# Optimization experiments

Hardware: AMD Instinct MI355X
Metric: run time of the kernel (lower is better)

The kernel has to match this reference:

```python
import jax, jax.numpy as jnp
import numpy as np

N_NODES = 10000
N_EDGES = 160000
N_GRAPHS = 16
NODE_F = 64
EDGE_F = 32
H = 256
OUT = 512
L = 3


def setup_inputs() -> dict:
    key = jax.random.key(0)
    ks = iter(jax.random.split(key, 64))
    def rn(shape, s=0.05):
        return jax.random.normal(next(ks), shape, dtype=jnp.float32) * s
    f32 = jnp.float32
    inp = {}
    inp["node_features"] = jax.random.normal(next(ks), (N_NODES, NODE_F), dtype=f32)
    inp["edge_index"] = jax.random.randint(next(ks), (2, N_EDGES), 0, N_NODES)
    inp["edge_features"] = jax.random.normal(next(ks), (N_EDGES, EDGE_F), dtype=f32)
    inp["batch"] = jnp.sort(jax.random.randint(next(ks), (N_NODES,), 0, N_GRAPHS))
    # node / edge embedding (Linear + LayerNorm)
    inp["node_w"] = rn((NODE_F, H)); inp["node_b"] = jnp.zeros((H,), f32)
    inp["node_g"] = jnp.ones((H,), f32); inp["node_beta"] = jnp.zeros((H,), f32)
    inp["edge_w"] = rn((EDGE_F, H)); inp["edge_b"] = jnp.zeros((H,), f32)
    inp["edge_g"] = jnp.ones((H,), f32); inp["edge_beta"] = jnp.zeros((H,), f32)
    # per-layer message MLP, GRUCell, LayerNorm (stacked over L layers)
    inp["mp_w1"] = rn((L, 3 * H, H)); inp["mp_b1"] = jnp.zeros((L, H), f32)
    inp["mp_w2"] = rn((L, H, H)); inp["mp_b2"] = jnp.zeros((L, H), f32)
    inp["gru_wih"] = rn((L, H, 3 * H)); inp["gru_whh"] = rn((L, H, 3 * H))
    inp["gru_bih"] = jnp.zeros((L, 3 * H), f32); inp["gru_bhh"] = jnp.zeros((L, 3 * H), f32)
    inp["mp_ln_g"] = jnp.ones((L, H), f32); inp["mp_ln_b"] = jnp.zeros((L, H), f32)
    # global attention pooling
    inp["att_w1"] = rn((H, H)); inp["att_b1"] = jnp.zeros((H,), f32)
    inp["att_w2"] = rn((H, 1)); inp["att_b2"] = jnp.zeros((1,), f32)
    # projection
    inp["proj_w"] = rn((H, OUT)); inp["proj_b"] = jnp.zeros((OUT,), f32)
    inp["proj_g"] = jnp.ones((OUT,), f32); inp["proj_beta"] = jnp.zeros((OUT,), f32)
    return inp


def _ln(x, g, b, eps=1e-5):
    m = x.mean(-1, keepdims=True)
    v = jnp.var(x, axis=-1, keepdims=True)
    return (x - m) / jnp.sqrt(v + eps) * g + b


def _forward(node_features, edge_index, edge_features, batch,
             node_w, node_b, node_g, node_beta,
             edge_w, edge_b, edge_g, edge_beta,
             mp_w1, mp_b1, mp_w2, mp_b2,
             gru_wih, gru_whh, gru_bih, gru_bhh,
             mp_ln_g, mp_ln_b,
             att_w1, att_b1, att_w2, att_b2,
             proj_w, proj_b, proj_g, proj_beta):
    src, dst = edge_index[0], edge_index[1]
    # node / edge embeddings (dropout is identity in eval)
    x = jax.nn.relu(_ln(node_features @ node_w + node_b, node_g, node_beta))
    edge_attr = jax.nn.relu(_ln(edge_features @ edge_w + edge_b, edge_g, edge_beta))
    n = x.shape[0]
    ones_e = jnp.ones((src.shape[0],), x.dtype)
    deg = jax.ops.segment_sum(ones_e, dst, num_segments=n)  # in-degree per node
    has_msg = (deg > 0)[:, None]
    for l in range(L):
        # messages: MLP(concat(src, dst, edge_attr))  [E, 3H] -> [E, H]
        m = jnp.concatenate([x[src], x[dst], edge_attr], axis=1)
        m = jax.nn.relu(m @ mp_w1[l] + mp_b1[l]) @ mp_w2[l] + mp_b2[l]
        # mean aggregation by destination node
        agg = jax.ops.segment_sum(m, dst, num_segments=n) / jnp.maximum(deg, 1.0)[:, None]
        # batched GRUCell update (torch gate order: r, z, n)
        gi = agg @ gru_wih[l] + gru_bih[l]
        gh = x @ gru_whh[l] + gru_bhh[l]
        r = jax.nn.sigmoid(gi[:, :H] + gh[:, :H])
        z = jax.nn.sigmoid(gi[:, H:2 * H] + gh[:, H:2 * H])
        ng = jnp.tanh(gi[:, 2 * H:] + r * gh[:, 2 * H:])
        h_new = (1.0 - z) * ng + z * x
        # nodes with no incoming edges keep old state, then LayerNorm over all
        x = _ln(jnp.where(has_msg, h_new, x), mp_ln_g[l], mp_ln_b[l])
    # global attention pooling: per-graph softmax over scores
    scores = jnp.tanh(x @ att_w1 + att_b1) @ att_w2 + att_b2  # [N, 1]
    s = scores[:, 0]
    smax = jax.ops.segment_max(s, batch, num_segments=N_GRAPHS)
    e = jnp.exp(s - smax[batch])
    denom = jax.ops.segment_sum(e, batch, num_segments=N_GRAPHS)
    w = e / denom[batch]
    pooled = jax.ops.segment_sum(x * w[:, None], batch, num_segments=N_GRAPHS)  # [B, H]
    return _ln(pooled @ proj_w + proj_b, proj_g, proj_beta)  # [B, OUT]


def reference(node_features, edge_index, edge_features, batch,
              node_w, node_b, node_g, node_beta,
              edge_w, edge_b, edge_g, edge_beta,
              mp_w1, mp_b1, mp_w2, mp_b2,
              gru_wih, gru_whh, gru_bih, gru_bhh,
              mp_ln_g, mp_ln_b,
              att_w1, att_b1, att_w2, att_b2,
              proj_w, proj_b, proj_g, proj_beta):
    return _forward(node_features, edge_index, edge_features, batch,
                    node_w, node_b, node_g, node_beta,
                    edge_w, edge_b, edge_g, edge_beta,
                    mp_w1, mp_b1, mp_w2, mp_b2,
                    gru_wih, gru_whh, gru_bih, gru_bhh,
                    mp_ln_g, mp_ln_b,
                    att_w1, att_b1, att_w2, att_b2,
                    proj_w, proj_b, proj_g, proj_beta)
```

## Files before the change

kernel.cpp:

```cpp
#include <hip/hip_runtime.h>

#define NN 10000
#define NE 160000
#define NG 16
#define NFD 64
#define EFD 32
#define H 256
#define OUTD 512
#define NL 3

typedef short v8s __attribute__((ext_vector_type(8)));
typedef float v4f __attribute__((ext_vector_type(4)));

__device__ __forceinline__ unsigned short f2bf(float f){
  unsigned int u = __float_as_uint(f);
  u = u + 0x7fffu + ((u >> 16) & 1u);
  return (unsigned short)(u >> 16);
}
__device__ __forceinline__ float bf2f(unsigned short u){
  return __uint_as_float(((unsigned int)u) << 16);
}

__global__ void node_enc(const float* __restrict__ nf, const float* __restrict__ W,
                         const float* __restrict__ b, const float* __restrict__ g,
                         const float* __restrict__ be,
                         float* __restrict__ x, unsigned short* __restrict__ xb){
  __shared__ float nfs[4][NFD];
  __shared__ float scr[16][2];
  int tid = threadIdx.x;
  int n0 = blockIdx.x * 4;
  { int n = tid >> 6, k = tid & 63; nfs[n][k] = nf[(n0 + n) * NFD + k]; }
  __syncthreads();
  float acc[4];
  float bb = b[tid];
  #pragma unroll
  for (int n = 0; n < 4; n++) acc[n] = bb;
  const float4* nfs4 = (const float4*)nfs;
  for (int kq = 0; kq < 16; kq++){
    float w0 = W[(kq * 4 + 0) * H + tid];
    float w1 = W[(kq * 4 + 1) * H + tid];
    float w2 = W[(kq * 4 + 2) * H + tid];
    float w3 = W[(kq * 4 + 3) * H + tid];
    #pragma unroll
    for (int n = 0; n < 4; n++){
      float4 e4 = nfs4[n * 16 + kq];
      acc[n] += e4.x * w0 + e4.y * w1 + e4.z * w2 + e4.w * w3;
    }
  }
  int lane = tid & 63, w = tid >> 6;
  float s1[4], s2[4];
  #pragma unroll
  for (int n = 0; n < 4; n++){
    s1[n] = acc[n]; s2[n] = acc[n] * acc[n];
    #pragma unroll
    for (int o = 32; o > 0; o >>= 1){
      s1[n] += __shfl_down(s1[n], o);
      s2[n] += __shfl_down(s2[n], o);
    }
  }
  if (lane == 0){
    #pragma unroll
    for (int n = 0; n < 4; n++){ scr[w * 4 + n][0] = s1[n]; scr[w * 4 + n][1] = s2[n]; }
  }
  __syncthreads();
  float gg = g[tid], bbe = be[tid];
  #pragma unroll
  for (int n = 0; n < 4; n++){
    float S1 = scr[n][0] + scr[4 + n][0] + scr[8 + n][0] + scr[12 + n][0];
    float S2 = scr[n][1] + scr[4 + n][1] + scr[8 + n][1] + scr[12 + n][1];
    float m = S1 / H, va = S2 / H - m * m;
    float y = (acc[n] - m) * rsqrtf(va + 1e-5f) * gg + bbe;
    y = fmaxf(y, 0.f);
    x[(size_t)(n0 + n) * H + tid] = y;
    xb[(size_t)(n0 + n) * H + tid] = f2bf(y);
  }
}

__global__ void edge_enc(const float* __restrict__ ef, const float* __restrict__ W,
                         const float* __restrict__ b, const float* __restrict__ g,
                         const float* __restrict__ be, unsigned short* __restrict__ eab){
  __shared__ float efs[8][EFD];
  __shared__ float scr[32][2];
  int tid = threadIdx.x;
  int e0 = blockIdx.x * 8;
  { int n = tid >> 5, k = tid & 31; efs[n][k] = ef[(e0 + n) * EFD + k]; }
  __syncthreads();
  float acc[8];
  float bb = b[tid];
  #pragma unroll
  for (int n = 0; n < 8; n++) acc[n] = bb;
  const float4* efs4 = (const float4*)efs;
  for (int kq = 0; kq < 8; kq++){
    float w0 = W[(kq * 4 + 0) * H + tid];
    float w1 = W[(kq * 4 + 1) * H + tid];
    float w2 = W[(kq * 4 + 2) * H + tid];
    float w3 = W[(kq * 4 + 3) * H + tid];
    #pragma unroll
    for (int n = 0; n < 8; n++){
      float4 e4 = efs4[n * 8 + kq];
      acc[n] += e4.x * w0 + e4.y * w1 + e4.z * w2 + e4.w * w3;
    }
  }
  int lane = tid & 63, w = tid >> 6;
  float s1[8], s2[8];
  #pragma unroll
  for (int n = 0; n < 8; n++){
    s1[n] = acc[n]; s2[n] = acc[n] * acc[n];
    #pragma unroll
    for (int o = 32; o > 0; o >>= 1){
      s1[n] += __shfl_down(s1[n], o);
      s2[n] += __shfl_down(s2[n], o);
    }
  }
  if (lane == 0){
    #pragma unroll
    for (int n = 0; n < 8; n++){ scr[w * 8 + n][0] = s1[n]; scr[w * 8 + n][1] = s2[n]; }
  }
  __syncthreads();
  float gg = g[tid], bbe = be[tid];
  #pragma unroll
  for (int n = 0; n < 8; n++){
    float S1 = scr[n][0] + scr[8 + n][0] + scr[16 + n][0] + scr[24 + n][0];
    float S2 = scr[n][1] + scr[8 + n][1] + scr[16 + n][1] + scr[24 + n][1];
    float m = S1 / H, va = S2 / H - m * m;
    float y = (acc[n] - m) * rsqrtf(va + 1e-5f) * gg + bbe;
    y = fmaxf(y, 0.f);
    eab[(size_t)(e0 + n) * H + tid] = f2bf(y);
  }
}

__global__ void hist_kernel(const int* __restrict__ dst, int* __restrict__ cnt){
  int e = blockIdx.x * 256 + threadIdx.x;
  if (e < NE) atomicAdd(&cnt[dst[e]], 1);
}

__global__ void scan_kernel(const int* __restrict__ cnt, int* __restrict__ start,
                            int* __restrict__ cursor){
  __shared__ int sums[256];
  int tid = threadIdx.x;
  const int PER = (NN + 255) / 256;
  int base = tid * PER;
  int s = 0;
  for (int i = 0; i < PER; i++){ int idx = base + i; if (idx < NN) s += cnt[idx]; }
  sums[tid] = s;
  __syncthreads();
  for (int o = 1; o < 256; o <<= 1){
    int t = (tid >= o) ? sums[tid - o] : 0;
    __syncthreads();
    sums[tid] += t;
    __syncthreads();
  }
  int run = sums[tid] - s;
  for (int i = 0; i < PER; i++){
    int idx = base + i;
    if (idx < NN){ start[idx] = run; cursor[idx] = run; run += cnt[idx]; }
  }
}

__global__ void place_kernel(const int* __restrict__ dst, int* __restrict__ cursor,
                             int* __restrict__ pos){
  int e = blockIdx.x * 256 + threadIdx.x;
  if (e < NE) pos[e] = atomicAdd(&cursor[dst[e]], 1);
}

__global__ void pack_w1(const float* __restrict__ w1, unsigned short* __restrict__ w1p){
  int b = blockIdx.x;
  int lane = threadIdx.x;
  int l = b / 384; int rem = b % 384; int kb = rem >> 4; int cb = rem & 15;
  const float* W = w1 + (size_t)l * 768 * H;
  unsigned short* out = w1p + ((size_t)b * 64 + lane) * 8;
  int col = cb * 16 + (lane & 15);
  int k0 = kb * 32 + 8 * (lane >> 4);
  #pragma unroll
  for (int i = 0; i < 8; i++) out[i] = f2bf(W[(size_t)(k0 + i) * H + col]);
}

__global__ void pack_w2t(const float* __restrict__ w2, unsigned short* __restrict__ w2tp){
  int b = blockIdx.x;
  int lane = threadIdx.x;
  int l = b / 128; int rem = b % 128; int hb = rem >> 3; int kb = rem & 7;
  const float* W = w2 + (size_t)l * H * H;
  unsigned short* out = w2tp + ((size_t)b * 64 + lane) * 8;
  int row = hb * 16 + (lane & 15);
  int k0 = kb * 32 + 8 * (lane >> 4);
  #pragma unroll
  for (int i = 0; i < 8; i++) out[i] = f2bf(W[(size_t)(k0 + i) * H + row]);
}

__global__ void pack_gruw(const float* __restrict__ wih, const float* __restrict__ whh,
                          unsigned short* __restrict__ gruw){
  int b = blockIdx.x;
  int lane = threadIdx.x;
  int l = b >> 10; int rem = b & 1023; int kb = rem >> 6; int cb = rem & 63;
  const float* WI = wih + (size_t)l * H * 768;
  const float* WH = whh + (size_t)l * H * 768;
  unsigned short* out = gruw + ((size_t)b * 64 + lane) * 8;
  int c = cb * 16 + (lane & 15);
  int r0 = kb * 32 + 8 * (lane >> 4);
  #pragma unroll
  for (int i = 0; i < 8; i++){
    int r = r0 + i;
    float v;
    if (r < 256) v = (c < 768) ? WI[(size_t)r * 768 + c] : 0.f;
    else         v = (c < 512) ? WH[(size_t)(r - 256) * 768 + c]
                               : ((c >= 768) ? WH[(size_t)(r - 256) * 768 + (c - 256)] : 0.f);
    out[i] = f2bf(v);
  }
}

__launch_bounds__(256)
__global__ void edge_mlp(const unsigned short* __restrict__ xb,
                         const unsigned short* __restrict__ eab,
                         const int* __restrict__ src, const int* __restrict__ dst,
                         const int* __restrict__ pos,
                         const unsigned short* __restrict__ w1p,
                         const float* __restrict__ b1,
                         const unsigned short* __restrict__ w2tp,
                         const float* __restrict__ b2,
                         unsigned short* __restrict__ m){
  __shared__ unsigned short As[64 * 64];
  __shared__ unsigned short C1s[64 * 256];
  __shared__ int srcs[64], dsts[64], poss[64];
  int tid = threadIdx.x;
  int e0 = blockIdx.x * 64;
  if (tid < 64){
    srcs[tid] = src[e0 + tid];
    dsts[tid] = dst[e0 + tid];
    poss[tid] = pos[e0 + tid];
  }
  int wave = tid >> 6, lane = tid & 63;
  int rl = lane & 15, q = lane >> 4;
  v4f acc[4][4];
  #pragma unroll
  for (int i = 0; i < 4; i++)
    #pragma unroll
    for (int j = 0; j < 4; j++) acc[i][j] = (v4f){0.f, 0.f, 0.f, 0.f};

  for (int kt = 0; kt < 12; ++kt){
    int seg = kt >> 2, off = (kt & 3) * 64;
    __syncthreads();
    #pragma unroll
    for (int h = 0; h < 2; ++h){
      int c = tid + h * 256;
      int e = c >> 3, ck = c & 7;
      const unsigned short* p;
      if (seg == 0)      p = xb + (size_t)srcs[e] * H;
      else if (seg == 1) p = xb + (size_t)dsts[e] * H;
      else               p = eab + (size_t)(e0 + e) * H;
      int4 v = *(const int4*)(p + off + ck * 8);
      *(int4*)&As[e * 64 + ((ck ^ (e & 7)) << 3)] = v;
    }
    __syncthreads();
    #pragma unroll
    for (int k2 = 0; k2 < 2; k2++){
      int kb = kt * 2 + k2;
      v8s af[4];
      #pragma unroll
      for (int rb = 0; rb < 4; rb++){
        int row = rb * 16 + rl;
        int ck = k2 * 4 + q;
        af[rb] = *(const v8s*)&As[row * 64 + ((ck ^ (row & 7)) << 3)];
      }
      #pragma unroll
      for (int cb = 0; cb < 4; cb++){
        v8s bf = *(const v8s*)&w1p[(((size_t)kb * 16 + (wave * 4 + cb)) * 64 + lane) * 8];
        #pragma unroll
        for (int rb = 0; rb < 4; rb++)
          acc[rb][cb] = __builtin_amdgcn_mfma_f32_16x16x32_bf16(af[rb], bf, acc[rb][cb], 0, 0, 0);
      }
    }
  }
  #pragma unroll
  for (int rb = 0; rb < 4; rb++){
    #pragma unroll
    for (int cb = 0; cb < 4; cb++){
      int col = wave * 64 + cb * 16 + rl;
      float bb = b1[col];
      #pragma unroll
      for (int j = 0; j < 4; j++){
        int row = rb * 16 + q * 4 + j;
        float v = fmaxf(acc[rb][cb][j] + bb, 0.f);
        C1s[row * 256 + (((col >> 3) ^ (row & 7)) << 3) + (col & 7)] = f2bf(v);
      }
    }
  }
  __syncthreads();
  v4f acc2[4][4];
  #pragma unroll
  for (int i = 0; i < 4; i++)
    #pragma unroll
    for (int j = 0; j < 4; j++) acc2[i][j] = (v4f){0.f, 0.f, 0.f, 0.f};
  #pragma unroll
  for (int kb = 0; kb < 8; kb++){
    v8s af[4];
    #pragma unroll
    for (int rb = 0; rb < 4; rb++)
      af[rb] = *(const v8s*)&w2tp[(((size_t)(wave * 4 + rb) * 8 + kb) * 64 + lane) * 8];
    #pragma unroll
    for (int cb = 0; cb < 4; cb++){
      int row = cb * 16 + rl;
      int ck = kb * 4 + q;
      v8s bf = *(const v8s*)&C1s[row * 256 + ((ck ^ (row & 7)) << 3)];
      #pragma unroll
      for (int rb = 0; rb < 4; rb++)
        acc2[rb][cb] = __builtin_amdgcn_mfma_f32_16x16x32_bf16(af[rb], bf, acc2[rb][cb], 0, 0, 0);
    }
  }
  #pragma unroll
  for (int cb = 0; cb < 4; cb++){
    int e = cb * 16 + rl;
    unsigned short* mrow = m + (size_t)poss[e] * H;
    #pragma unroll
    for (int rb = 0; rb < 4; rb++){
      int oc0 = wave * 64 + rb * 16 + q * 4;
      ushort4 v;
      v.x = f2bf(acc2[rb][cb][0] + b2[oc0 + 0]);
      v.y = f2bf(acc2[rb][cb][1] + b2[oc0 + 1]);
      v.z = f2bf(acc2[rb][cb][2] + b2[oc0 + 2]);
      v.w = f2bf(acc2[rb][cb][3] + b2[oc0 + 3]);
      *(ushort4*)&mrow[oc0] = v;
    }
  }
}

__global__ void agg_kernel(const unsigned short* __restrict__ m,
                           const int* __restrict__ start, const int* __restrict__ cnt,
                           unsigned short* __restrict__ aggb){
  int node = blockIdx.x * 4 + (threadIdx.x >> 6);
  int lane = threadIdx.x & 63;
  int s0 = start[node], d = cnt[node];
  float a0 = 0.f, a1 = 0.f, a2 = 0.f, a3 = 0.f;
  const unsigned short* base = m + (size_t)s0 * H + lane * 4;
  for (int r = 0; r < d; r++){
    ushort4 v = *(const ushort4*)(base + (size_t)r * H);
    a0 += bf2f(v.x); a1 += bf2f(v.y); a2 += bf2f(v.z); a3 += bf2f(v.w);
  }
  float inv = 1.f / fmaxf((float)d, 1.f);
  ushort4 o;
  o.x = f2bf(a0 * inv); o.y = f2bf(a1 * inv); o.z = f2bf(a2 * inv); o.w = f2bf(a3 * inv);
  *(ushort4*)&aggb[(size_t)node * H + lane * 4] = o;
}

__launch_bounds__(512)
__global__ void gates_gemm(const unsigned short* __restrict__ aggb,
                           const unsigned short* __restrict__ xb,
                           const unsigned short* __restrict__ gruw,
                           float* __restrict__ gates){
  __shared__ unsigned short As[32 * 64];
  int tid = threadIdx.x;
  int n0 = blockIdx.x * 32;
  int wave = tid >> 6, lane = tid & 63;
  int rl = lane & 15, q = lane >> 4;
  v4f acc[2][8];
  #pragma unroll
  for (int i = 0; i < 2; i++)
    #pragma unroll
    for (int j = 0; j < 8; j++) acc[i][j] = (v4f){0.f, 0.f, 0.f, 0.f};

  for (int kt = 0; kt < 8; kt++){
    __syncthreads();
    if (tid < 256){
      int e = tid >> 3, ck = tid & 7;
      int n = n0 + e; if (n >= NN) n = NN - 1;
      const unsigned short* p = (kt < 4) ? (aggb + (size_t)n * H + kt * 64)
                                         : (xb   + (size_t)n * H + (kt - 4) * 64);
      int4 v = *(const int4*)(p + ck * 8);
      *(int4*)&As[e * 64 + ((ck ^ (e & 7)) << 3)] = v;
    }
    __syncthreads();
    #pragma unroll
    for (int ks = 0; ks < 2; ks++){
      int kb = kt * 2 + ks;
      v8s af[2];
      #pragma unroll
      for (int rb = 0; rb < 2; rb++){
        int row = rb * 16 + rl;
        int ck = ks * 4 + q;
        af[rb] = *(const v8s*)&As[row * 64 + ((ck ^ (row & 7)) << 3)];
      }
      #pragma unroll
      for (int cb = 0; cb < 8; cb++){
        v8s bf = *(const v8s*)&gruw[(((size_t)kb * 64 + (wave * 8 + cb)) * 64 + lane) * 8];
        #pragma unroll
        for (int rb = 0; rb < 2; rb++)
          acc[rb][cb] = __builtin_amdgcn_mfma_f32_16x16x32_bf16(af[rb], bf, acc[rb][cb], 0, 0, 0);
      }
    }
  }
  #pragma unroll
  for (int rb = 0; rb < 2; rb++){
    #pragma unroll
    for (int cb = 0; cb < 8; cb++){
      int col = wave * 128 + cb * 16 + rl;
      #pragma unroll
      for (int j = 0; j < 4; j++){
        int row = n0 + rb * 16 + q * 4 + j;
        if (row < NN) gates[(size_t)row * 1024 + col] = acc[rb][cb][j];
      }
    }
  }
}

__global__ void gru_elem(const float* __restrict__ gates, const int* __restrict__ cnt,
                         float* __restrict__ x, unsigned short* __restrict__ xb,
                         const float* __restrict__ bih, const float* __restrict__ bhh,
                         const float* __restrict__ lng, const float* __restrict__ lnb){
  __shared__ float scr[16][2];
  __shared__ float dgs[4];
  int tid = threadIdx.x;
  int n0 = blockIdx.x * 4;
  if (tid < 4) dgs[tid] = (float)cnt[n0 + tid];
  __syncthreads();
  float bir = bih[tid], biz = bih[256 + tid], bin = bih[512 + tid];
  float bhr = bhh[tid], bhz = bhh[256 + tid], bhn = bhh[512 + tid];
  float h[4];
  #pragma unroll
  for (int n = 0; n < 4; n++){
    const float* gp = gates + (size_t)(n0 + n) * 1024;
    float rs = gp[tid], zs = gp[256 + tid], gin = gp[512 + tid], ghn = gp[768 + tid];
    float xv = x[(size_t)(n0 + n) * H + tid];
    float r  = 1.f / (1.f + __expf(-(rs + bir + bhr)));
    float z  = 1.f / (1.f + __expf(-(zs + biz + bhz)));
    float ng = tanhf(gin + bin + r * (ghn + bhn));
    float hn = (1.f - z) * ng + z * xv;
    h[n] = (dgs[n] > 0.f) ? hn : xv;
  }
  int lane = tid & 63, w = tid >> 6;
  float s1[4], s2[4];
  #pragma unroll
  for (int n = 0; n < 4; n++){
    s1[n] = h[n]; s2[n] = h[n] * h[n];
    #pragma unroll
    for (int o = 32; o > 0; o >>= 1){
      s1[n] += __shfl_down(s1[n], o);
      s2[n] += __shfl_down(s2[n], o);
    }
  }
  if (lane == 0){
    #pragma unroll
    for (int n = 0; n < 4; n++){ scr[w * 4 + n][0] = s1[n]; scr[w * 4 + n][1] = s2[n]; }
  }
  __syncthreads();
  float gg = lng[tid], bb = lnb[tid];
  #pragma unroll
  for (int n = 0; n < 4; n++){
    float S1 = scr[n][0] + scr[4 + n][0] + scr[8 + n][0] + scr[12 + n][0];
    float S2 = scr[n][1] + scr[4 + n][1] + scr[8 + n][1] + scr[12 + n][1];
    float m = S1 / H, va = S2 / H - m * m;
    float y = (h[n] - m) * rsqrtf(va + 1e-5f) * gg + bb;
    x[(size_t)(n0 + n) * H + tid] = y;
    xb[(size_t)(n0 + n) * H + tid] = f2bf(y);
  }
}

__global__ void scores_kernel(const float* __restrict__ x, const float* __restrict__ w1,
                              const float* __restrict__ b1, const float* __restrict__ w2,
                              const float* __restrict__ b2, float* __restrict__ s){
  __shared__ float xs[4][H];
  __shared__ float scr[16];
  int tid = threadIdx.x;
  int n0 = blockIdx.x * 4;
  for (int idx = tid; idx < 4 * H; idx += 256){
    int n = idx >> 8, k = idx & 255;
    xs[n][k] = x[(size_t)(n0 + n) * H + k];
  }
  __syncthreads();
  float acc[4];
  float bb = b1[tid];
  #pragma unroll
  for (int n = 0; n < 4; n++) acc[n] = bb;
  const float4* xs4 = (const float4*)xs;
  for (int kq = 0; kq < 64; kq++){
    float w0 = w1[(kq * 4 + 0) * H + tid];
    float w1v = w1[(kq * 4 + 1) * H + tid];
    float w2v = w1[(kq * 4 + 2) * H + tid];
    float w3 = w1[(kq * 4 + 3) * H + tid];
    #pragma unroll
    for (int n = 0; n < 4; n++){
      float4 e4 = xs4[n * 64 + kq];
      acc[n] += e4.x * w0 + e4.y * w1v + e4.z * w2v + e4.w * w3;
    }
  }
  float wv = w2[tid];
  int lane = tid & 63, w = tid >> 6;
  float t[4];
  #pragma unroll
  for (int n = 0; n < 4; n++){
    t[n] = tanhf(acc[n]) * wv;
    #pragma unroll
    for (int o = 32; o > 0; o >>= 1) t[n] += __shfl_down(t[n], o);
  }
  if (lane == 0){
    #pragma unroll
    for (int n = 0; n < 4; n++) scr[w * 4 + n] = t[n];
  }
  __syncthreads();
  if (tid < 4) s[n0 + tid] = scr[tid] + scr[4 + tid] + scr[8 + tid] + scr[12 + tid] + b2[0];
}

__global__ void pool_kernel(const float* __restrict__ x, const float* __restrict__ s,
                            const int* __restrict__ batch, float* __restrict__ pooled){
  __shared__ float scr[8];
  int g = blockIdx.x, tid = threadIdx.x;
  int a = 0, b = NN;
  while (a < b){ int mid = (a + b) >> 1; if (batch[mid] < g) a = mid + 1; else b = mid; }
  int lo = a;
  a = lo; b = NN;
  while (a < b){ int mid = (a + b) >> 1; if (batch[mid] < g + 1) a = mid + 1; else b = mid; }
  int hi = a;
  float mx = -3.4e38f;
  for (int i = lo + tid; i < hi; i += 256) mx = fmaxf(mx, s[i]);
  #pragma unroll
  for (int o = 32; o > 0; o >>= 1) mx = fmaxf(mx, __shfl_down(mx, o));
  int lane = tid & 63, w = tid >> 6;
  __syncthreads();
  if (lane == 0) scr[w] = mx;
  __syncthreads();
  mx = fmaxf(fmaxf(scr[0], scr[1]), fmaxf(scr[2], scr[3]));
  float den = 0.f;
  for (int i = lo + tid; i < hi; i += 256) den += __expf(s[i] - mx);
  #pragma unroll
  for (int o = 32; o > 0; o >>= 1) den += __shfl_down(den, o);
  __syncthreads();
  if (lane == 0) scr[4 + w] = den;
  __syncthreads();
  den = scr[4] + scr[5] + scr[6] + scr[7];
  float pj = 0.f;
  for (int i = lo; i < hi; i++){
    float wgt = __expf(s[i] - mx);
    pj += wgt * x[(size_t)i * H + tid];
  }
  pooled[g * H + tid] = pj / den;
}

__global__ void proj_kernel(const float* __restrict__ pooled, const float* __restrict__ W,
                            const float* __restrict__ b, const float* __restrict__ g,
                            const float* __restrict__ be, float* __restrict__ out){
  __shared__ float ps[H];
  __shared__ float scr[8];
  int gi = blockIdx.x, tid = threadIdx.x;
  ps[tid] = pooled[gi * H + tid];
  __syncthreads();
  float a0 = b[tid], a1 = b[tid + 256];
  for (int k = 0; k < H; k++){
    float p = ps[k];
    a0 += p * W[k * OUTD + tid];
    a1 += p * W[k * OUTD + tid + 256];
  }
  float s1 = a0 + a1, s2 = a0 * a0 + a1 * a1;
  int lane = tid & 63, w = tid >> 6;
  #pragma unroll
  for (int o = 32; o > 0; o >>= 1){
    s1 += __shfl_down(s1, o);
    s2 += __shfl_down(s2, o);
  }
  __syncthreads();
  if (lane == 0){ scr[w] = s1; scr[4 + w] = s2; }
  __syncthreads();
  s1 = scr[0] + scr[1] + scr[2] + scr[3];
  s2 = scr[4] + scr[5] + scr[6] + scr[7];
  float m = s1 / OUTD, va = s2 / OUTD - m * m;
  float rs = rsqrtf(va + 1e-5f);
  out[gi * OUTD + tid]       = (a0 - m) * rs * g[tid] + be[tid];
  out[gi * OUTD + tid + 256] = (a1 - m) * rs * g[tid + 256] + be[tid + 256];
}

extern "C" void kernel_launch(void* const* d_in, const int* in_sizes, int n_in,
                              void* d_out, int out_size, void* d_ws, size_t ws_size,
                              hipStream_t stream){
  const float* nf        = (const float*)d_in[0];
  const int*   eidx      = (const int*)d_in[1];
  const float* ef        = (const float*)d_in[2];
  const int*   batch     = (const int*)d_in[3];
  const float* node_w    = (const float*)d_in[4];
  const float* node_b    = (const float*)d_in[5];
  const float* node_g    = (const float*)d_in[6];
  const float* node_beta = (const float*)d_in[7];
  const float* edge_w    = (const float*)d_in[8];
  const float* edge_b    = (const float*)d_in[9];
  const float* edge_g    = (const float*)d_in[10];
  const float* edge_beta = (const float*)d_in[11];
  const float* mp_w1     = (const float*)d_in[12];
  const float* mp_b1     = (const float*)d_in[13];
  const float* mp_w2     = (const float*)d_in[14];
  const float* mp_b2     = (const float*)d_in[15];
  const float* gru_wih   = (const float*)d_in[16];
  const float* gru_whh   = (const float*)d_in[17];
  const float* gru_bih   = (const float*)d_in[18];
  const float* gru_bhh   = (const float*)d_in[19];
  const float* mp_ln_g   = (const float*)d_in[20];
  const float* mp_ln_b   = (const float*)d_in[21];
  const float* att_w1    = (const float*)d_in[22];
  const float* att_b1    = (const float*)d_in[23];
  const float* att_w2    = (const float*)d_in[24];
  const float* att_b2    = (const float*)d_in[25];
  const float* proj_w    = (const float*)d_in[26];
  const float* proj_b    = (const float*)d_in[27];
  const float* proj_g    = (const float*)d_in[28];
  const float* proj_beta = (const float*)d_in[29];
  const int* src = eidx;
  const int* dst = eidx + NE;

  char* ws = (char*)d_ws;
  size_t off = 0;
  auto alloc = [&](size_t bytes) -> void* {
    void* p = ws + off;
    off += (bytes + 511) & ~(size_t)511;
    return p;
  };
  float*          x      = (float*)alloc((size_t)NN * H * 4);
  unsigned short* xb     = (unsigned short*)alloc((size_t)NN * H * 2);
  unsigned short* eab    = (unsigned short*)alloc((size_t)NE * H * 2);
  unsigned short* m      = (unsigned short*)alloc((size_t)NE * H * 2);
  unsigned short* aggb   = (unsigned short*)alloc((size_t)NN * H * 2);
  int*            cnt    = (int*)alloc((size_t)NN * 4);
  int*            startA = (int*)alloc((size_t)NN * 4);
  int*            cursor = (int*)alloc((size_t)NN * 4);
  int*            pos    = (int*)alloc((size_t)NE * 4);
  float*          s      = (float*)alloc((size_t)NN * 4);
  float*          pooled = (float*)alloc((size_t)NG * H * 4);
  unsigned short* w1p    = (unsigned short*)alloc((size_t)3 * 24 * 16 * 64 * 8 * 2);
  unsigned short* w2tp   = (unsigned short*)alloc((size_t)3 * 16 * 8 * 64 * 8 * 2);
  unsigned short* gruw   = (unsigned short*)alloc((size_t)3 * 16 * 64 * 64 * 8 * 2);
  float*          gates  = (float*)m;

  hipMemsetAsync(cnt, 0, (size_t)NN * 4, stream);
  hist_kernel<<<(NE + 255) / 256, 256, 0, stream>>>(dst, cnt);
  scan_kernel<<<1, 256, 0, stream>>>(cnt, startA, cursor);
  place_kernel<<<(NE + 255) / 256, 256, 0, stream>>>(dst, cursor, pos);

  pack_w1<<<1152, 64, 0, stream>>>(mp_w1, w1p);
  pack_w2t<<<384, 64, 0, stream>>>(mp_w2, w2tp);
  pack_gruw<<<3072, 64, 0, stream>>>(gru_wih, gru_whh, gruw);
  node_enc<<<NN / 4, 256, 0, stream>>>(nf, node_w, node_b, node_g, node_beta, x, xb);
  edge_enc<<<NE / 8, 256, 0, stream>>>(ef, edge_w, edge_b, edge_g, edge_beta, eab);

  for (int l = 0; l < NL; l++){
    edge_mlp<<<NE / 64, 256, 0, stream>>>(xb, eab, src, dst, pos,
        w1p + (size_t)l * 24 * 16 * 64 * 8, mp_b1 + l * H,
        w2tp + (size_t)l * 16 * 8 * 64 * 8, mp_b2 + l * H, m);
    agg_kernel<<<NN / 4, 256, 0, stream>>>(m, startA, cnt, aggb);
    gates_gemm<<<(NN + 31) / 32, 512, 0, stream>>>(aggb, xb,
        gruw + (size_t)l * 16 * 64 * 64 * 8, gates);
    gru_elem<<<NN / 4, 256, 0, stream>>>(gates, cnt, x, xb,
        gru_bih + l * 768, gru_bhh + l * 768,
        mp_ln_g + l * H, mp_ln_b + l * H);
  }
  scores_kernel<<<NN / 4, 256, 0, stream>>>(x, att_w1, att_b1, att_w2, att_b2, s);
  pool_kernel<<<NG, 256, 0, stream>>>(x, s, batch, pooled);
  proj_kernel<<<NG, 256, 0, stream>>>(pooled, proj_w, proj_b, proj_g, proj_beta, (float*)d_out);
  (void)in_sizes; (void)n_in; (void)out_size; (void)ws_size;
}
```

Baseline: 1.432 ms.

## Double-buffer edge_mlp A tiles with register prefetch of next gathered chunk

The edge MLP's first GEMM now uses two shared-memory A buffers and prefetches the next k-tile's gathered rows (src, dst or edge-attribute) into registers while MFMAs run on the current tile. This removes one barrier per k iteration and hides the gather latency behind compute. In exchange it costs an extra 8KB of LDS and more live registers, which may lower occupancy.

```diff
diff --git a/kernel.cpp b/kernel.cpp
--- a/kernel.cpp
+++ b/kernel.cpp
@@ -218,7 +218,7 @@
                          const unsigned short* __restrict__ w2tp,
                          const float* __restrict__ b2,
                          unsigned short* __restrict__ m){
-  __shared__ unsigned short As[64 * 64];
+  __shared__ unsigned short As[2][64 * 64];
   __shared__ unsigned short C1s[64 * 256];
   __shared__ int srcs[64], dsts[64], poss[64];
   int tid = threadIdx.x;
@@ -230,6 +230,19 @@
   }
   int wave = tid >> 6, lane = tid & 63;
   int rl = lane & 15, q = lane >> 4;
+  int eA = tid >> 3, eB = 32 + eA, ckk = tid & 7;
+  int swA = eA * 64 + ((ckk ^ (eA & 7)) << 3);
+  int swB = eB * 64 + ((ckk ^ (eB & 7)) << 3);
+  __syncthreads();
+
+  int4 r0, r1;
+  {
+    const unsigned short* p0 = xb + (size_t)srcs[eA] * H;
+    const unsigned short* p1 = xb + (size_t)srcs[eB] * H;
+    r0 = *(const int4*)(p0 + ckk * 8);
+    r1 = *(const int4*)(p1 + ckk * 8);
+  }
+
   v4f acc[4][4];
   #pragma unroll
   for (int i = 0; i < 4; i++)
@@ -237,20 +250,20 @@
     for (int j = 0; j < 4; j++) acc[i][j] = (v4f){0.f, 0.f, 0.f, 0.f};
 
   for (int kt = 0; kt < 12; ++kt){
-    int seg = kt >> 2, off = (kt & 3) * 64;
+    unsigned short* Ab = As[kt & 1];
+    *(int4*)&Ab[swA] = r0;
+    *(int4*)&Ab[swB] = r1;
     __syncthreads();
-    #pragma unroll
-    for (int h = 0; h < 2; ++h){
-      int c = tid + h * 256;
-      int e = c >> 3, ck = c & 7;
-      const unsigned short* p;
-      if (seg == 0)      p = xb + (size_t)srcs[e] * H;
-      else if (seg == 1) p = xb + (size_t)dsts[e] * H;
-      else               p = eab + (size_t)(e0 + e) * H;
-      int4 v = *(const int4*)(p + off + ck * 8);
-      *(int4*)&As[e * 64 + ((ck ^ (e & 7)) << 3)] = v;
-    }
-    __syncthreads();
+    if (kt < 11){
+      int kn = kt + 1;
+      int seg = kn >> 2, off = (kn & 3) * 64;
+      const unsigned short *p0, *p1;
+      if (seg == 0){      p0 = xb + (size_t)srcs[eA] * H; p1 = xb + (size_t)srcs[eB] * H; }
+      else if (seg == 1){ p0 = xb + (size_t)dsts[eA] * H; p1 = xb + (size_t)dsts[eB] * H; }
+      else {              p0 = eab + (size_t)(e0 + eA) * H; p1 = eab + (size_t)(e0 + eB) * H; }
+      r0 = *(const int4*)(p0 + off + ckk * 8);
+      r1 = *(const int4*)(p1 + off + ckk * 8);
+    }
     #pragma unroll
     for (int k2 = 0; k2 < 2; k2++){
       int kb = kt * 2 + k2;
@@ -259,7 +272,7 @@
       for (int rb = 0; rb < 4; rb++){
         int row = rb * 16 + rl;
         int ck = k2 * 4 + q;
-        af[rb] = *(const v8s*)&As[row * 64 + ((ck ^ (row & 7)) << 3)];
+        af[rb] = *(const v8s*)&Ab[row * 64 + ((ck ^ (row & 7)) << 3)];
       }
       #pragma unroll
       for (int cb = 0; cb < 4; cb++){
```

Result: faster. 1.321 ms (-7.8%).
